# Optimization experiments

Hardware: AMD Instinct MI355X
Metric: run time of the kernel (lower is better)

Reference implementation:

```python
import jax, jax.numpy as jnp
import numpy as np

BN_EPS = 1e-5


def setup_inputs() -> dict:
    key = jax.random.key(0)
    ks = jax.random.split(key, 8)
    B, C, H, W = 2, 512, 64, 64
    Ck, Cv = 256, 256
    x = jax.random.normal(ks[0], (B, C, H, W), jnp.float32)
    # f_key/f_query shared 1x1 conv (kaiming, relu)
    wk = jax.random.normal(ks[1], (Ck, C), jnp.float32) * (2.0 / C) ** 0.5
    bk = jnp.zeros((Ck,), jnp.float32)
    bn_gamma = jax.random.uniform(ks[2], (Ck,), jnp.float32, 0.5, 1.5)
    bn_beta = jax.random.normal(ks[3], (Ck,), jnp.float32) * 0.1
    bn_mean = jax.random.normal(ks[4], (Ck,), jnp.float32) * 0.1
    bn_var = jax.random.uniform(ks[5], (Ck,), jnp.float32, 0.5, 1.5)
    # f_value: 3x3 conv then 1x1 conv
    wv1 = jax.random.normal(ks[6], (Cv, C, 3, 3), jnp.float32) * (2.0 / (C * 9)) ** 0.5
    bv1 = jnp.zeros((Cv,), jnp.float32)
    wv2 = jax.random.normal(ks[7], (Cv, Cv), jnp.float32) * (2.0 / Cv) ** 0.5
    bv2 = jnp.zeros((Cv,), jnp.float32)
    return dict(x=x, wk=wk, bk=bk, bn_gamma=bn_gamma, bn_beta=bn_beta,
                bn_mean=bn_mean, bn_var=bn_var, wv1=wv1, bv1=bv1, wv2=wv2, bv2=bv2)


def reference(x, wk, bk, bn_gamma, bn_beta, bn_mean, bn_var, wv1, bv1, wv2, bv2):
    B, C, H, W = x.shape
    Ck, Cv = wk.shape[0], wv1.shape[0]
    N = H * W
    # f_key == f_query: 1x1 conv + BN (inference form) + ReLU
    feat = jnp.einsum('oc,bchw->bohw', wk, x) + bk[:, None, None]
    scale_bn = (bn_gamma / jnp.sqrt(bn_var + BN_EPS))
    feat = (feat - bn_mean[:, None, None]) * scale_bn[:, None, None] + bn_beta[:, None, None]
    feat = jax.nn.relu(feat).reshape(B, Ck, N)  # [B, Ck, N]
    # sim_map = softmax(Ck^-0.5 * Q^T K); Q and K are the same tensor
    sim_map = jax.nn.softmax(jnp.einsum('bcn,bcm->bnm', feat, feat) * (Ck ** -0.5), axis=-1)
    # f_value: conv3x3 + relu + conv1x1 + relu
    v = jax.lax.conv_general_dilated(x, wv1, (1, 1), 'SAME',
                                     dimension_numbers=('NCHW', 'OIHW', 'NCHW'))
    v = jax.nn.relu(v + bv1[:, None, None])
    v = jax.nn.relu(jnp.einsum('oc,bchw->bohw', wv2, v) + bv2[:, None, None])
    v = v.reshape(B, Cv, N)  # [B, Cv, N]
    context = jnp.einsum('bnm,bcm->bcn', sim_map, v).reshape(B, Cv, H, W)
    return context, sim_map
```

## Files before the change

kernel.cpp:

```cpp
#include <hip/hip_runtime.h>
#include <hip/hip_bf16.h>
#include <stdint.h>

typedef unsigned short u16_t;
typedef __attribute__((ext_vector_type(8))) short short8;
typedef __attribute__((ext_vector_type(4))) float f32x4;
typedef __attribute__((ext_vector_type(4))) unsigned short us4;

__device__ __forceinline__ float bf2f(u16_t u) {
  union { unsigned int i; float f; } c; c.i = ((unsigned int)u) << 16; return c.f;
}
__device__ __forceinline__ u16_t f2bf(float f) {
  union { float f; unsigned int i; } c; c.f = f;
  unsigned int x = c.i;
  unsigned int r = x + 0x7fffu + ((x >> 16) & 1u);
  return (u16_t)(r >> 16);
}

__device__ __forceinline__ void gload_lds16(const u16_t* g, u16_t* l) {
  __builtin_amdgcn_global_load_lds(
      (const __attribute__((address_space(1))) void*)g,
      (__attribute__((address_space(3))) void*)(unsigned int)(uintptr_t)l,
      16, 0, 0);
}

struct Seg {
  const u16_t* Ah;
  const u16_t* Al;
  const u16_t* Bh;
  const u16_t* Bl;
  int boff;
};

struct GemmArgs {
  Seg segs[9];
  int nseg;
  int segs_per_split;
  int K;
  int ldA, ldB;
  long long sA, sB;
  float alpha;
  float* outf;
  long long sOut;
  long long sSplit;
  int ldT;
};

template<int BM, int BN, int MODE, bool PADB, bool SYMM>
__global__ __launch_bounds__(256, 4) void gemm_tn(GemmArgs args) {
  constexpr int FM = BM / 32, FN = BN / 32;
  constexpr int AH_E = 4 * BM * 8;
  constexpr int AL_E = (MODE == 0) ? 4 * BM * 8 : 8;
  constexpr int BH_E = 4 * BN * 8;
  constexpr int BL_E = (MODE <= 1) ? 4 * BN * 8 : 8;
  constexpr int SM_E = AH_E + AL_E + BH_E + BL_E;
  static_assert(!SYMM || (size_t)SM_E * 2 >= 32 * 132 * 4, "tbuf alias too small");
  __shared__ __align__(16) u16_t smem[SM_E];
  u16_t* aflat_h = smem;
  u16_t* aflat_l = smem + AH_E;
  u16_t* bflat_h = smem + AH_E + AL_E;
  u16_t* bflat_l = smem + AH_E + AL_E + BH_E;

  const int tid = threadIdx.x;
  const int wave = tid >> 6, lane = tid & 63;
  const int lhi = lane >> 4, llo = lane & 15;
  const int wr = wave >> 1, wc = wave & 1;
  int nt, mt, b, split;
  if (SYMM) {
    b = blockIdx.z; split = 0;
    int t = blockIdx.x, r = 0;
    while (t >= 32 - r) { t -= 32 - r; ++r; }
    mt = r; nt = r + t;
  } else {
    nt = blockIdx.x; mt = blockIdx.y;
    b = blockIdx.z & 1; split = blockIdx.z >> 1;
  }
  const int row0 = mt * BM, col0 = nt * BN;

  f32x4 acc[FM][FN];
  const f32x4 zero4 = {0.f, 0.f, 0.f, 0.f};
#pragma unroll
  for (int i = 0; i < FM; ++i)
#pragma unroll
    for (int j = 0; j < FN; ++j) acc[i][j] = zero4;

  constexpr int RA = BM / 64;
  constexpr int RB = BN / 64;

  const int s0 = split * args.segs_per_split;
  int s1 = s0 + args.segs_per_split;
  if (s1 > args.nseg) s1 = args.nseg;

  for (int s = s0; s < s1; ++s) {
    const u16_t* Abh = args.segs[s].Ah + (size_t)b * args.sA;
    const u16_t* Abl = args.segs[s].Al + (size_t)b * args.sA;
    const u16_t* Bbh = args.segs[s].Bh + (size_t)b * args.sB;
    const u16_t* Bbl = args.segs[s].Bl + (size_t)b * args.sB;
    const int boff = args.segs[s].boff;
    for (int k0 = 0; k0 < args.K; k0 += 32) {
      __syncthreads();
#pragma unroll
      for (int r = 0; r < RA; ++r) {
        int idx = (r * 4 + wave) * 64 + lane;
        int chunk = idx / BM, m = idx % BM;
        size_t goff = (size_t)(row0 + m) * args.ldA + (k0 + chunk * 8);
        gload_lds16(Abh + goff, aflat_h + (size_t)((r * 4 + wave) * 64) * 8);
        if (MODE == 0)
          gload_lds16(Abl + goff, aflat_l + (size_t)((r * 4 + wave) * 64) * 8);
      }
#pragma unroll
      for (int r = 0; r < RB; ++r) {
        int idx = (r * 4 + wave) * 64 + lane;
        int chunk = idx / BN, n = idx % BN;
        long long rowi;
        if (PADB) {
          int gn = col0 + n;
          rowi = (long long)((gn >> 6) + 1) * 66 + (gn & 63) + 1 + boff;
        } else {
          rowi = col0 + n;
        }
        size_t goff = (size_t)rowi * args.ldB + (k0 + chunk * 8);
        gload_lds16(Bbh + goff, bflat_h + (size_t)((r * 4 + wave) * 64) * 8);
        if (MODE <= 1)
          gload_lds16(Bbl + goff, bflat_l + (size_t)((r * 4 + wave) * 64) * 8);
      }
      __syncthreads();
      short8 afh[FM], afl[FM], bfh[FN], bfl[FN];
#pragma unroll
      for (int i = 0; i < FM; ++i) {
        afh[i] = *(const short8*)(aflat_h + ((size_t)lhi * BM + wr * (BM / 2) + i * 16 + llo) * 8);
        if (MODE == 0)
          afl[i] = *(const short8*)(aflat_l + ((size_t)lhi * BM + wr * (BM / 2) + i * 16 + llo) * 8);
      }
#pragma unroll
      for (int j = 0; j < FN; ++j) {
        bfh[j] = *(const short8*)(bflat_h + ((size_t)lhi * BN + wc * (BN / 2) + j * 16 + llo) * 8);
        if (MODE <= 1)
          bfl[j] = *(const short8*)(bflat_l + ((size_t)lhi * BN + wc * (BN / 2) + j * 16 + llo) * 8);
      }
#pragma unroll
      for (int i = 0; i < FM; ++i)
#pragma unroll
        for (int j = 0; j < FN; ++j) {
          f32x4 t = acc[i][j];
          if (MODE <= 1)
            t = __builtin_amdgcn_mfma_f32_16x16x32_bf16(afh[i], bfl[j], t, 0, 0, 0);
          if (MODE == 0)
            t = __builtin_amdgcn_mfma_f32_16x16x32_bf16(afl[i], bfh[j], t, 0, 0, 0);
          t = __builtin_amdgcn_mfma_f32_16x16x32_bf16(afh[i], bfh[j], t, 0, 0, 0);
          acc[i][j] = t;
        }
    }
  }

  float* outp = args.outf + (size_t)split * args.sSplit + (size_t)b * args.sOut;
#pragma unroll
  for (int i = 0; i < FM; ++i) {
    int mb = row0 + wr * (BM / 2) + i * 16 + lhi * 4;
#pragma unroll
    for (int j = 0; j < FN; ++j) {
      int n = col0 + wc * (BN / 2) + j * 16 + llo;
      f32x4 vv = acc[i][j] * args.alpha;
      *(f32x4*)(outp + (size_t)n * args.ldT + mb) = vv;
    }
  }
  if (SYMM) {
    if (nt != mt) {
      float* tb = (float*)smem;
#pragma unroll
      for (int i = 0; i < FM; ++i) {
        __syncthreads();
#pragma unroll
        for (int j = 0; j < FN; ++j) {
#pragma unroll
          for (int r2 = 0; r2 < 4; ++r2) {
            int trow = wr * 16 + lhi * 4 + r2;
            int tcol = wc * 64 + j * 16 + llo;
            tb[trow * 132 + tcol] = acc[i][j][r2] * args.alpha;
          }
        }
        __syncthreads();
#pragma unroll
        for (int it = 0; it < 4; ++it) {
          int idx = it * 256 + tid;
          int row = idx >> 5, c4 = idx & 31;
          int mg = row0 + (row >> 4) * 64 + i * 16 + (row & 15);
          f32x4 v4 = *(f32x4*)&tb[row * 132 + c4 * 4];
          *(f32x4*)(outp + (size_t)mg * args.ldT + col0 + c4 * 4) = v4;
        }
      }
    }
  }
}

__global__ __launch_bounds__(256) void zeropad(u16_t* __restrict__ xh, u16_t* __restrict__ xl) {
  int rowi = blockIdx.x % 260;
  int b = blockIdx.x / 260;
  int rp;
  if (rowi < 66) rp = rowi;
  else if (rowi < 132) rp = 4290 + (rowi - 66);
  else { int g = (rowi - 132) >> 1; rp = (g + 1) * 66 + ((rowi - 132) & 1) * 65; }
  size_t base = ((size_t)b * 4356 + rp) * 512;
  int t = threadIdx.x;
  const us4 z = {0, 0, 0, 0};
  if (t < 128) *(us4*)(xh + base + (size_t)t * 4) = z;
  else *(us4*)(xl + base + (size_t)(t - 128) * 4) = z;
}

template<int LDT, bool PER_COL>
__global__ __launch_bounds__(256) void reduce_split(
    const float* __restrict__ part, long long sSplit, int ns,
    const float* __restrict__ scale, const float* __restrict__ bias,
    u16_t* __restrict__ oh, u16_t* __restrict__ ol, long long total) {
  long long i = ((long long)blockIdx.x * 256 + threadIdx.x) * 4;
  if (i >= total) return;
  f32x4 s = *(const f32x4*)(part + i);
  for (int p = 1; p < ns; ++p) s += *(const f32x4*)(part + (size_t)p * sSplit + i);
  f32x4 v;
  if (PER_COL) {
    int c = (int)(i & (LDT - 1));
    f32x4 bi = *(const f32x4*)(bias + c);
    if (scale) { f32x4 sc = *(const f32x4*)(scale + c); v = s * sc + bi; }
    else v = s + bi;
  } else {
    int r = (int)((i / LDT) & 255);
    float bi = bias[r];
    v = s + bi;
  }
  us4 h, l;
#pragma unroll
  for (int c2 = 0; c2 < 4; ++c2) {
    float vv = v[c2] > 0.f ? v[c2] : 0.f;
    u16_t hh = f2bf(vv);
    h[c2] = hh;
    l[c2] = f2bf(vv - bf2f(hh));
  }
  *(us4*)(oh + i) = h;
  if (ol) *(us4*)(ol + i) = l;
}

__global__ __launch_bounds__(256) void reduce_split_f32(
    const float* __restrict__ part, long long sSplit, int ns,
    float* __restrict__ out, long long total) {
  long long i = ((long long)blockIdx.x * 256 + threadIdx.x) * 4;
  if (i >= total) return;
  f32x4 s = *(const f32x4*)(part + i);
  for (int p = 1; p < ns; ++p) s += *(const f32x4*)(part + (size_t)p * sSplit + i);
  *(f32x4*)(out + i) = s;
}

__global__ __launch_bounds__(256) void softmax_k(float* S, u16_t* P) {
  const int row = blockIdx.x;
  float* Sr = S + (size_t)row * 4096;
  u16_t* Pr = P + (size_t)row * 4096;
  const int t = threadIdx.x;
  const int wave = t >> 6;
  f32x4 v[4];
  float vmax = -3.4e38f;
#pragma unroll
  for (int i = 0; i < 4; ++i) {
    v[i] = ((const f32x4*)Sr)[t + i * 256];
#pragma unroll
    for (int c = 0; c < 4; ++c) vmax = fmaxf(vmax, v[i][c]);
  }
#pragma unroll
  for (int off = 32; off; off >>= 1) vmax = fmaxf(vmax, __shfl_xor(vmax, off));
  __shared__ float red[4];
  if ((t & 63) == 0) red[wave] = vmax;
  __syncthreads();
  vmax = fmaxf(fmaxf(red[0], red[1]), fmaxf(red[2], red[3]));
  float sum = 0.f;
#pragma unroll
  for (int i = 0; i < 4; ++i)
#pragma unroll
    for (int c = 0; c < 4; ++c) { v[i][c] = __expf(v[i][c] - vmax); sum += v[i][c]; }
#pragma unroll
  for (int off = 32; off; off >>= 1) sum += __shfl_xor(sum, off);
  __shared__ float red2[4];
  if ((t & 63) == 0) red2[wave] = sum;
  __syncthreads();
  sum = red2[0] + red2[1] + red2[2] + red2[3];
  float rs = 1.0f / sum;
#pragma unroll
  for (int i = 0; i < 4; ++i) {
    f32x4 o = v[i] * rs;
    ((f32x4*)Sr)[t + i * 256] = o;
    us4 pb;
#pragma unroll
    for (int c = 0; c < 4; ++c) pb[c] = f2bf(o[c]);
    ((us4*)Pr)[t + i * 256] = pb;
  }
}

__global__ __launch_bounds__(256) void xprep(const float* __restrict__ x,
                                             u16_t* __restrict__ xh, u16_t* __restrict__ xl) {
  __shared__ float tile[64][65];
  const int b = blockIdx.z, c0 = blockIdx.y * 64, n0 = blockIdx.x * 64;
  const float* xb = x + ((size_t)b * 512 + c0) * 4096 + n0;
  const int t = threadIdx.x;
  const int tr = t >> 6, tc = t & 63;
#pragma unroll
  for (int rr = 0; rr < 16; ++rr) {
    int ci = tr + rr * 4;
    tile[ci][tc] = xb[(size_t)ci * 4096 + tc];
  }
  __syncthreads();
#pragma unroll
  for (int rr = 0; rr < 16; ++rr) {
    int nj = rr * 4 + tr;
    float v = tile[tc][nj];
    size_t rp = (size_t)(blockIdx.x + 1) * 66 + nj + 1;
    size_t o = ((size_t)b * 4356 + rp) * 512 + c0 + tc;
    u16_t hh = f2bf(v);
    xh[o] = hh;
    xl[o] = f2bf(v - bf2f(hh));
  }
}

__global__ __launch_bounds__(256) void prep_all(
    const float* __restrict__ wk, const float* __restrict__ wv2, const float* __restrict__ wv1,
    const float* __restrict__ g, const float* __restrict__ be, const float* __restrict__ mu,
    const float* __restrict__ var, const float* __restrict__ bkb,
    u16_t* __restrict__ wkh, u16_t* __restrict__ wkl,
    u16_t* __restrict__ w2h, u16_t* __restrict__ w2l,
    u16_t* __restrict__ w1h, float* __restrict__ bnA, float* __restrict__ bnB) {
  long long i = (long long)blockIdx.x * 256 + threadIdx.x;
  if (i < 256) {
    float s = g[i] * rsqrtf(var[i] + 1e-5f);
    bnA[i] = s;
    bnB[i] = (bkb[i] - mu[i]) * s + be[i];
    return;
  }
  i -= 256;
  if (i < 131072) {
    float v = wk[i];
    u16_t hh = f2bf(v);
    wkh[i] = hh; wkl[i] = f2bf(v - bf2f(hh));
    return;
  }
  i -= 131072;
  if (i < 65536) {
    float v = wv2[i];
    u16_t hh = f2bf(v);
    w2h[i] = hh; w2l[i] = f2bf(v - bf2f(hh));
    return;
  }
  i -= 65536;
  if (i < 1179648) {
    int tp = (int)(i / (256 * 512));
    int rem = (int)(i % (256 * 512));
    int o = rem / 512, c = rem % 512;
    w1h[i] = f2bf(wv1[((size_t)o * 512 + c) * 9 + tp]);
  }
}

extern "C" void kernel_launch(void* const* d_in, const int* in_sizes, int n_in,
                              void* d_out, int out_size, void* d_ws, size_t ws_size,
                              hipStream_t stream) {
  (void)in_sizes; (void)n_in; (void)out_size; (void)ws_size;
  const float* x   = (const float*)d_in[0];
  const float* wk  = (const float*)d_in[1];
  const float* bk  = (const float*)d_in[2];
  const float* gam = (const float*)d_in[3];
  const float* bet = (const float*)d_in[4];
  const float* mu  = (const float*)d_in[5];
  const float* var = (const float*)d_in[6];
  const float* wv1 = (const float*)d_in[7];
  const float* bv1 = (const float*)d_in[8];
  const float* wv2 = (const float*)d_in[9];
  const float* bv2 = (const float*)d_in[10];

  const int B = 2;
  const size_t XT_E  = (size_t)B * 4356 * 512;
  const size_t WK_E  = 256 * 512;
  const size_t WV1_E = 9ull * 256 * 512;
  const size_t WV2_E = 256 * 256;
  const size_t FT_E  = (size_t)B * 4096 * 256;
  const size_t P_E   = (size_t)B * 4096 * 4096;

  size_t off = 0;
  auto carve = [&](size_t bytes) -> char* {
    off = (off + 255) & ~(size_t)255;
    char* p = (char*)d_ws + off;
    off += bytes;
    return p;
  };
  u16_t* xh  = (u16_t*)carve(XT_E * 2);
  u16_t* xl  = (u16_t*)carve(XT_E * 2);
  u16_t* wkh = (u16_t*)carve(WK_E * 2);
  u16_t* wkl = (u16_t*)carve(WK_E * 2);
  u16_t* w1h = (u16_t*)carve(WV1_E * 2);
  u16_t* w1l = (u16_t*)carve(WV1_E * 2);
  u16_t* w2h = (u16_t*)carve(WV2_E * 2);
  u16_t* w2l = (u16_t*)carve(WV2_E * 2);
  u16_t* fth = (u16_t*)carve(FT_E * 2);
  u16_t* ftl = (u16_t*)carve(FT_E * 2);
  u16_t* v1h = (u16_t*)carve(FT_E * 2);
  u16_t* v1l = (u16_t*)carve(FT_E * 2);
  u16_t* vh  = (u16_t*)carve(FT_E * 2);
  u16_t* vl  = (u16_t*)carve(FT_E * 2);
  u16_t* Pb  = (u16_t*)carve(P_E * 2);
  float* bnA = (float*)carve(256 * 4);
  float* bnB = (float*)carve(256 * 4);

  float* big_part = (float*)Pb;
  float* pv_part  = (float*)d_ws;

  float* ctx = (float*)d_out;
  float* sim = (float*)d_out + (size_t)B * 256 * 4096;

  const long long FT_LL = (long long)FT_E;

  zeropad<<<520, 256, 0, stream>>>(xh, xl);
  prep_all<<<5377, 256, 0, stream>>>(wk, wv2, wv1, gam, bet, mu, var, bk,
                                     wkh, wkl, w2h, w2l, w1h, bnA, bnB);
  xprep<<<dim3(64, 8, 2), 256, 0, stream>>>(x, xh, xl);

  {
    GemmArgs a = {};
    a.segs[0] = {wkh,       wkl,       xh,       xl,       0};
    a.segs[1] = {wkh + 256, wkl + 256, xh + 256, xl + 256, 0};
    a.nseg = 2; a.segs_per_split = 1; a.K = 256; a.ldA = 512; a.ldB = 512;
    a.sA = 0; a.sB = (long long)4356 * 512; a.alpha = 1.f;
    a.outf = big_part; a.sOut = (long long)4096 * 256; a.sSplit = FT_LL; a.ldT = 256;
    gemm_tn<64, 128, 0, true, false><<<dim3(32, 4, 4), 256, 0, stream>>>(a);
    reduce_split<256, true><<<2048, 256, 0, stream>>>(big_part, FT_LL, 2, bnA, bnB, fth, ftl, FT_LL);
  }
  {
    GemmArgs a = {};
    a.segs[0] = {fth, nullptr, fth, ftl, 0};
    a.nseg = 1; a.segs_per_split = 1; a.K = 256; a.ldA = 256; a.ldB = 256;
    a.sA = (long long)4096 * 256; a.sB = (long long)4096 * 256; a.alpha = 0.0625f;
    a.outf = sim; a.sOut = (long long)4096 * 4096; a.sSplit = 0; a.ldT = 4096;
    gemm_tn<128, 128, 1, false, true><<<dim3(528, 1, 2), 256, 0, stream>>>(a);
  }
  {
    GemmArgs a = {};
    for (int ty = 0; ty < 3; ++ty)
      for (int tx = 0; tx < 3; ++tx) {
        int tp = ty * 3 + tx;
        int boff = (ty - 1) * 66 + (tx - 1);
        a.segs[tp] = {w1h + (size_t)tp * 131072, nullptr, xh, nullptr, boff};
      }
    a.nseg = 9; a.segs_per_split = 2; a.K = 512; a.ldA = 512; a.ldB = 512;
    a.sA = 0; a.sB = (long long)4356 * 512; a.alpha = 1.f;
    a.outf = big_part; a.sOut = (long long)4096 * 256; a.sSplit = FT_LL; a.ldT = 256;
    gemm_tn<128, 128, 2, true, false><<<dim3(32, 2, 10), 256, 0, stream>>>(a);
    reduce_split<256, true><<<2048, 256, 0, stream>>>(big_part, FT_LL, 5, nullptr, bv1, v1h, v1l, FT_LL);
  }
  {
    GemmArgs a = {};
    a.segs[0] = {v1h,       v1l,       w2h,       w2l,       0};
    a.segs[1] = {v1h + 128, v1l + 128, w2h + 128, w2l + 128, 0};
    a.nseg = 2; a.segs_per_split = 1; a.K = 128; a.ldA = 256; a.ldB = 256;
    a.sA = (long long)4096 * 256; a.sB = 0; a.alpha = 1.f;
    a.outf = big_part; a.sOut = (long long)256 * 4096; a.sSplit = FT_LL; a.ldT = 4096;
    gemm_tn<128, 64, 0, false, false><<<dim3(4, 32, 4), 256, 0, stream>>>(a);
    reduce_split<4096, false><<<2048, 256, 0, stream>>>(big_part, FT_LL, 2, nullptr, bv2, vh, nullptr, FT_LL);
  }
  softmax_k<<<B * 4096, 256, 0, stream>>>(sim, Pb);
  {
    GemmArgs a = {};
    for (int q = 0; q < 4; ++q)
      a.segs[q] = {Pb + (size_t)q * 1024, nullptr, vh + (size_t)q * 1024, nullptr, 0};
    a.nseg = 4; a.segs_per_split = 1; a.K = 1024; a.ldA = 4096; a.ldB = 4096;
    a.sA = (long long)4096 * 4096; a.sB = (long long)256 * 4096; a.alpha = 1.f;
    a.outf = pv_part; a.sOut = (long long)256 * 4096; a.sSplit = FT_LL; a.ldT = 4096;
    gemm_tn<128, 128, 2, false, false><<<dim3(2, 32, 8), 256, 0, stream>>>(a);
    reduce_split_f32<<<2048, 256, 0, stream>>>(pv_part, FT_LL, 4, ctx, FT_LL);
  }
  (void)vl; (void)w1l;
}
```

Before: 281.1 us.

## Add dedicated conv3x3 GEMM reusing shared input tile across horizontal taps

Replaces the 9-segment split-K conv3x3 GEMM with a kernel where each block handles one kernel row and loads a single padded input strip (144 rows) into LDS. All three horizontal taps reuse that strip via shifted LDS reads, which cuts global input traffic and shrinks the partial-sum reduction from 5 splits to 3. It also folds the zero-pad kernel into the prep kernel to save a launch, and doubles the K-chunk depth per LDS stage for the P·V GEMM to halve barriers per K. The costs are more LDS per block for the P·V GEMM, and the conv kernel relies on hard-coded shapes.

```diff
diff --git a/kernel.cpp b/kernel.cpp
--- a/kernel.cpp
+++ b/kernel.cpp
@@ -46,13 +46,13 @@
   int ldT;
 };
 
-template<int BM, int BN, int MODE, bool PADB, bool SYMM>
+template<int BM, int BN, int MODE, bool PADB, bool SYMM, int NCH = 4>
 __global__ __launch_bounds__(256, 4) void gemm_tn(GemmArgs args) {
   constexpr int FM = BM / 32, FN = BN / 32;
-  constexpr int AH_E = 4 * BM * 8;
-  constexpr int AL_E = (MODE == 0) ? 4 * BM * 8 : 8;
-  constexpr int BH_E = 4 * BN * 8;
-  constexpr int BL_E = (MODE <= 1) ? 4 * BN * 8 : 8;
+  constexpr int AH_E = NCH * BM * 8;
+  constexpr int AL_E = (MODE == 0) ? NCH * BM * 8 : 8;
+  constexpr int BH_E = NCH * BN * 8;
+  constexpr int BL_E = (MODE <= 1) ? NCH * BN * 8 : 8;
   constexpr int SM_E = AH_E + AL_E + BH_E + BL_E;
   static_assert(!SYMM || (size_t)SM_E * 2 >= 32 * 132 * 4, "tbuf alias too small");
   __shared__ __align__(16) u16_t smem[SM_E];
@@ -84,8 +84,8 @@
 #pragma unroll
     for (int j = 0; j < FN; ++j) acc[i][j] = zero4;
 
-  constexpr int RA = BM / 64;
-  constexpr int RB = BN / 64;
+  constexpr int RA = BM * NCH / 256;
+  constexpr int RB = BN * NCH / 256;
 
   const int s0 = split * args.segs_per_split;
   int s1 = s0 + args.segs_per_split;
@@ -97,20 +97,20 @@
     const u16_t* Bbh = args.segs[s].Bh + (size_t)b * args.sB;
     const u16_t* Bbl = args.segs[s].Bl + (size_t)b * args.sB;
     const int boff = args.segs[s].boff;
-    for (int k0 = 0; k0 < args.K; k0 += 32) {
+    for (int k0 = 0; k0 < args.K; k0 += NCH * 8) {
       __syncthreads();
 #pragma unroll
       for (int r = 0; r < RA; ++r) {
-        int idx = (r * 4 + wave) * 64 + lane;
+        int idx = r * 256 + tid;
         int chunk = idx / BM, m = idx % BM;
         size_t goff = (size_t)(row0 + m) * args.ldA + (k0 + chunk * 8);
-        gload_lds16(Abh + goff, aflat_h + (size_t)((r * 4 + wave) * 64) * 8);
+        gload_lds16(Abh + goff, aflat_h + (size_t)idx * 8);
         if (MODE == 0)
-          gload_lds16(Abl + goff, aflat_l + (size_t)((r * 4 + wave) * 64) * 8);
+          gload_lds16(Abl + goff, aflat_l + (size_t)idx * 8);
       }
 #pragma unroll
       for (int r = 0; r < RB; ++r) {
-        int idx = (r * 4 + wave) * 64 + lane;
+        int idx = r * 256 + tid;
         int chunk = idx / BN, n = idx % BN;
         long long rowi;
         if (PADB) {
@@ -120,36 +120,41 @@
           rowi = col0 + n;
         }
         size_t goff = (size_t)rowi * args.ldB + (k0 + chunk * 8);
-        gload_lds16(Bbh + goff, bflat_h + (size_t)((r * 4 + wave) * 64) * 8);
+        gload_lds16(Bbh + goff, bflat_h + (size_t)idx * 8);
         if (MODE <= 1)
-          gload_lds16(Bbl + goff, bflat_l + (size_t)((r * 4 + wave) * 64) * 8);
+          gload_lds16(Bbl + goff, bflat_l + (size_t)idx * 8);
       }
       __syncthreads();
-      short8 afh[FM], afl[FM], bfh[FN], bfl[FN];
-#pragma unroll
-      for (int i = 0; i < FM; ++i) {
-        afh[i] = *(const short8*)(aflat_h + ((size_t)lhi * BM + wr * (BM / 2) + i * 16 + llo) * 8);
-        if (MODE == 0)
-          afl[i] = *(const short8*)(aflat_l + ((size_t)lhi * BM + wr * (BM / 2) + i * 16 + llo) * 8);
+#pragma unroll
+      for (int kk = 0; kk < NCH / 4; ++kk) {
+        const int ckA = (kk * 4 + lhi) * BM;
+        const int ckB = (kk * 4 + lhi) * BN;
+        short8 afh[FM], afl[FM], bfh[FN], bfl[FN];
+#pragma unroll
+        for (int i = 0; i < FM; ++i) {
+          afh[i] = *(const short8*)(aflat_h + ((size_t)ckA + wr * (BM / 2) + i * 16 + llo) * 8);
+          if (MODE == 0)
+            afl[i] = *(const short8*)(aflat_l + ((size_t)ckA + wr * (BM / 2) + i * 16 + llo) * 8);
+        }
+#pragma unroll
+        for (int j = 0; j < FN; ++j) {
+          bfh[j] = *(const short8*)(bflat_h + ((size_t)ckB + wc * (BN / 2) + j * 16 + llo) * 8);
+          if (MODE <= 1)
+            bfl[j] = *(const short8*)(bflat_l + ((size_t)ckB + wc * (BN / 2) + j * 16 + llo) * 8);
+        }
+#pragma unroll
+        for (int i = 0; i < FM; ++i)
+#pragma unroll
+          for (int j = 0; j < FN; ++j) {
+            f32x4 t = acc[i][j];
+            if (MODE <= 1)
+              t = __builtin_amdgcn_mfma_f32_16x16x32_bf16(afh[i], bfl[j], t, 0, 0, 0);
+            if (MODE == 0)
+              t = __builtin_amdgcn_mfma_f32_16x16x32_bf16(afl[i], bfh[j], t, 0, 0, 0);
+            t = __builtin_amdgcn_mfma_f32_16x16x32_bf16(afh[i], bfh[j], t, 0, 0, 0);
+            acc[i][j] = t;
+          }
       }
-#pragma unroll
-      for (int j = 0; j < FN; ++j) {
-        bfh[j] = *(const short8*)(bflat_h + ((size_t)lhi * BN + wc * (BN / 2) + j * 16 + llo) * 8);
-        if (MODE <= 1)
-          bfl[j] = *(const short8*)(bflat_l + ((size_t)lhi * BN + wc * (BN / 2) + j * 16 + llo) * 8);
-      }
-#pragma unroll
-      for (int i = 0; i < FM; ++i)
-#pragma unroll
-        for (int j = 0; j < FN; ++j) {
-          f32x4 t = acc[i][j];
-          if (MODE <= 1)
-            t = __builtin_amdgcn_mfma_f32_16x16x32_bf16(afh[i], bfl[j], t, 0, 0, 0);
-          if (MODE == 0)
-            t = __builtin_amdgcn_mfma_f32_16x16x32_bf16(afl[i], bfh[j], t, 0, 0, 0);
-          t = __builtin_amdgcn_mfma_f32_16x16x32_bf16(afh[i], bfh[j], t, 0, 0, 0);
-          acc[i][j] = t;
-        }
     }
   }
 
@@ -193,18 +198,86 @@
   }
 }
 
-__global__ __launch_bounds__(256) void zeropad(u16_t* __restrict__ xh, u16_t* __restrict__ xl) {
-  int rowi = blockIdx.x % 260;
-  int b = blockIdx.x / 260;
-  int rp;
-  if (rowi < 66) rp = rowi;
-  else if (rowi < 132) rp = 4290 + (rowi - 66);
-  else { int g = (rowi - 132) >> 1; rp = (g + 1) * 66 + ((rowi - 132) & 1) * 65; }
-  size_t base = ((size_t)b * 4356 + rp) * 512;
-  int t = threadIdx.x;
-  const us4 z = {0, 0, 0, 0};
-  if (t < 128) *(us4*)(xh + base + (size_t)t * 4) = z;
-  else *(us4*)(xl + base + (size_t)(t - 128) * 4) = z;
+struct Conv3Args {
+  const u16_t* W;
+  const u16_t* X;
+  float* outf;
+  long long sOut;
+  long long sSplit;
+};
+__global__ __launch_bounds__(256, 4) void conv3_gemm(Conv3Args a) {
+  __shared__ __align__(16) u16_t lA[3][4][128][8];
+  __shared__ __align__(16) u16_t lB[4 * 144 * 8];
+  const int tid = threadIdx.x;
+  const int wave = tid >> 6, lane = tid & 63;
+  const int lhi = lane >> 4, llo = lane & 15;
+  const int wr = wave >> 1, wc = wave & 1;
+  const int nt = blockIdx.x, mt = blockIdx.y;
+  const int b = blockIdx.z & 1, ty = blockIdx.z >> 1;
+  const int row0 = mt * 128;
+  const int base = (2 * nt + ty) * 66;
+  const u16_t* Xb = a.X + (size_t)b * 4356 * 512;
+  const u16_t* Wt = a.W + (size_t)(ty * 3) * 131072;
+
+  f32x4 acc[4][4];
+  const f32x4 zero4 = {0.f, 0.f, 0.f, 0.f};
+#pragma unroll
+  for (int i = 0; i < 4; ++i)
+#pragma unroll
+    for (int j = 0; j < 4; ++j) acc[i][j] = zero4;
+
+  for (int k0 = 0; k0 < 512; k0 += 32) {
+    __syncthreads();
+#pragma unroll
+    for (int t = 0; t < 3; ++t)
+#pragma unroll
+      for (int r = 0; r < 2; ++r) {
+        int slot = r * 256 + tid;
+        int chunk = slot >> 7, m = slot & 127;
+        const u16_t* src = Wt + (size_t)t * 131072 + (size_t)(row0 + m) * 512 + k0 + chunk * 8;
+        gload_lds16(src, &lA[t][0][0][0] + (size_t)slot * 8);
+      }
+#pragma unroll
+    for (int r = 0; r < 2; ++r) {
+      int idx = r * 256 + tid;
+      int chunk = idx / 144, rr = idx % 144;
+      gload_lds16(Xb + (size_t)(base + rr) * 512 + k0 + chunk * 8, lB + (size_t)idx * 8);
+    }
+    if (tid < 64) {
+      int idx = 512 + tid;
+      int chunk = idx / 144, rr = idx % 144;
+      gload_lds16(Xb + (size_t)(base + rr) * 512 + k0 + chunk * 8, lB + (size_t)idx * 8);
+    }
+    __syncthreads();
+#pragma unroll
+    for (int t = 0; t < 3; ++t) {
+      short8 af[4], bf[4];
+#pragma unroll
+      for (int i = 0; i < 4; ++i)
+        af[i] = *(const short8*)&lA[t][lhi][wr * 64 + i * 16 + llo][0];
+#pragma unroll
+      for (int j = 0; j < 4; ++j) {
+        int rB = wc * 66 + j * 16 + llo + t;
+        bf[j] = *(const short8*)(lB + ((size_t)lhi * 144 + rB) * 8);
+      }
+#pragma unroll
+      for (int i = 0; i < 4; ++i)
+#pragma unroll
+        for (int j = 0; j < 4; ++j)
+          acc[i][j] = __builtin_amdgcn_mfma_f32_16x16x32_bf16(af[i], bf[j], acc[i][j], 0, 0, 0);
+    }
+  }
+
+  float* outp = a.outf + (size_t)ty * a.sSplit + (size_t)b * a.sOut;
+#pragma unroll
+  for (int i = 0; i < 4; ++i) {
+    int mb = row0 + wr * 64 + i * 16 + lhi * 4;
+#pragma unroll
+    for (int j = 0; j < 4; ++j) {
+      int n = (nt << 7) + wc * 64 + j * 16 + llo;
+      *(f32x4*)(outp + (size_t)n * 256 + mb) = acc[i][j];
+    }
+  }
 }
 
 template<int LDT, bool PER_COL>
@@ -323,7 +396,8 @@
     const float* __restrict__ var, const float* __restrict__ bkb,
     u16_t* __restrict__ wkh, u16_t* __restrict__ wkl,
     u16_t* __restrict__ w2h, u16_t* __restrict__ w2l,
-    u16_t* __restrict__ w1h, float* __restrict__ bnA, float* __restrict__ bnB) {
+    u16_t* __restrict__ w1h, float* __restrict__ bnA, float* __restrict__ bnB,
+    u16_t* __restrict__ xh, u16_t* __restrict__ xl) {
   long long i = (long long)blockIdx.x * 256 + threadIdx.x;
   if (i < 256) {
     float s = g[i] * rsqrtf(var[i] + 1e-5f);
@@ -351,6 +425,20 @@
     int rem = (int)(i % (256 * 512));
     int o = rem / 512, c = rem % 512;
     w1h[i] = f2bf(wv1[((size_t)o * 512 + c) * 9 + tp]);
+    return;
+  }
+  i -= 1179648;
+  if (i < 133120) {
+    int blk = (int)(i >> 8), t = (int)(i & 255);
+    int rowi = blk % 260, b = blk / 260;
+    int rp;
+    if (rowi < 66) rp = rowi;
+    else if (rowi < 132) rp = 4290 + (rowi - 66);
+    else { int g2 = (rowi - 132) >> 1; rp = (g2 + 1) * 66 + ((rowi - 132) & 1) * 65; }
+    size_t base = ((size_t)b * 4356 + rp) * 512;
+    const us4 z = {0, 0, 0, 0};
+    if (t < 128) *(us4*)(xh + base + (size_t)t * 4) = z;
+    else *(us4*)(xl + base + (size_t)(t - 128) * 4) = z;
   }
 }
 
@@ -390,7 +478,6 @@
   u16_t* wkh = (u16_t*)carve(WK_E * 2);
   u16_t* wkl = (u16_t*)carve(WK_E * 2);
   u16_t* w1h = (u16_t*)carve(WV1_E * 2);
-  u16_t* w1l = (u16_t*)carve(WV1_E * 2);
   u16_t* w2h = (u16_t*)carve(WV2_E * 2);
   u16_t* w2l = (u16_t*)carve(WV2_E * 2);
   u16_t* fth = (u16_t*)carve(FT_E * 2);
@@ -398,7 +485,6 @@
   u16_t* v1h = (u16_t*)carve(FT_E * 2);
   u16_t* v1l = (u16_t*)carve(FT_E * 2);
   u16_t* vh  = (u16_t*)carve(FT_E * 2);
-  u16_t* vl  = (u16_t*)carve(FT_E * 2);
   u16_t* Pb  = (u16_t*)carve(P_E * 2);
   float* bnA = (float*)carve(256 * 4);
   float* bnB = (float*)carve(256 * 4);
@@ -411,9 +497,8 @@
 
   const long long FT_LL = (long long)FT_E;
 
-  zeropad<<<520, 256, 0, stream>>>(xh, xl);
-  prep_all<<<5377, 256, 0, stream>>>(wk, wv2, wv1, gam, bet, mu, var, bk,
-                                     wkh, wkl, w2h, w2l, w1h, bnA, bnB);
+  prep_all<<<5897, 256, 0, stream>>>(wk, wv2, wv1, gam, bet, mu, var, bk,
+                                     wkh, wkl, w2h, w2l, w1h, bnA, bnB, xh, xl);
   xprep<<<dim3(64, 8, 2), 256, 0, stream>>>(x, xh, xl);
 
   {
@@ -435,18 +520,11 @@
     gemm_tn<128, 128, 1, false, true><<<dim3(528, 1, 2), 256, 0, stream>>>(a);
   }
   {
-    GemmArgs a = {};
-    for (int ty = 0; ty < 3; ++ty)
-      for (int tx = 0; tx < 3; ++tx) {
-        int tp = ty * 3 + tx;
-        int boff = (ty - 1) * 66 + (tx - 1);
-        a.segs[tp] = {w1h + (size_t)tp * 131072, nullptr, xh, nullptr, boff};
-      }
-    a.nseg = 9; a.segs_per_split = 2; a.K = 512; a.ldA = 512; a.ldB = 512;
-    a.sA = 0; a.sB = (long long)4356 * 512; a.alpha = 1.f;
-    a.outf = big_part; a.sOut = (long long)4096 * 256; a.sSplit = FT_LL; a.ldT = 256;
-    gemm_tn<128, 128, 2, true, false><<<dim3(32, 2, 10), 256, 0, stream>>>(a);
-    reduce_split<256, true><<<2048, 256, 0, stream>>>(big_part, FT_LL, 5, nullptr, bv1, v1h, v1l, FT_LL);
+    Conv3Args a;
+    a.W = w1h; a.X = xh;
+    a.outf = big_part; a.sOut = (long long)4096 * 256; a.sSplit = FT_LL;
+    conv3_gemm<<<dim3(32, 2, 6), 256, 0, stream>>>(a);
+    reduce_split<256, true><<<2048, 256, 0, stream>>>(big_part, FT_LL, 3, nullptr, bv1, v1h, v1l, FT_LL);
   }
   {
     GemmArgs a = {};
@@ -466,8 +544,7 @@
     a.nseg = 4; a.segs_per_split = 1; a.K = 1024; a.ldA = 4096; a.ldB = 4096;
     a.sA = (long long)4096 * 4096; a.sB = (long long)256 * 4096; a.alpha = 1.f;
     a.outf = pv_part; a.sOut = (long long)256 * 4096; a.sSplit = FT_LL; a.ldT = 4096;
-    gemm_tn<128, 128, 2, false, false><<<dim3(2, 32, 8), 256, 0, stream>>>(a);
+    gemm_tn<128, 128, 2, false, false, 8><<<dim3(2, 32, 8), 256, 0, stream>>>(a);
     reduce_split_f32<<<2048, 256, 0, stream>>>(pv_part, FT_LL, 4, ctx, FT_LL);
   }
-  (void)vl; (void)w1l;
-}
+}
```

New measurement: 265.9 us. 1.06x faster.
